# Kernel tuning notes

Measured on AMD Instinct MI355X. Metric: run time of the kernel, lower is better.

The kernel has to match this reference:

```python
import jax, jax.numpy as jnp
import numpy as np

B_, NWIN, WH, WW = 8, 256, 8, 8
DIM, HEADS = 192, 6
N = WH * WW


def setup_inputs() -> dict:
    key = jax.random.key(0)
    ks = jax.random.split(key, 5)
    return {
        "x": jax.random.normal(ks[0], (B_, NWIN, N, DIM), dtype=jnp.float32),
        "qkv_w": jax.random.normal(ks[1], (3 * DIM, DIM), dtype=jnp.float32) * 0.02,
        "qkv_b": jax.random.normal(ks[2], (3 * DIM,), dtype=jnp.float32) * 0.02,
        "proj_w": jax.random.normal(ks[3], (DIM, DIM), dtype=jnp.float32) * 0.02,
        "proj_b": jax.random.normal(ks[4], (DIM,), dtype=jnp.float32) * 0.02,
    }


def _grad_magnitude(t, B, H, n, d, Wh, Ww):
    # t: [B,H,n,N,d] -> spatial layout [B,H,n,d,Wh,Ww]
    t = jnp.swapaxes(t, 3, 4).reshape(B, H, n, d, Wh, Ww)
    # forward finite difference with zero pre-pad (matches conv2d [-1,1] pad=1 then slice)
    gx = t - jnp.concatenate([jnp.zeros_like(t[..., :1]), t[..., :-1]], axis=-1)
    gy = t - jnp.concatenate([jnp.zeros_like(t[..., :1, :]), t[..., :-1, :]], axis=-2)
    return jnp.sum(jnp.abs(gx) + jnp.abs(gy), axis=(-1, -2))  # [B,H,n,d]


def reference(x, qkv_w, qkv_b, proj_w, proj_b):
    B, n, Ntok, C = x.shape
    H = HEADS
    d = C // H
    scale = d ** (-0.5)
    qkv = x @ qkv_w.T + qkv_b                       # [B,n,N,3C]
    qkv = qkv.reshape(B, n, Ntok, 3, H, d)
    qkv = jnp.transpose(qkv, (3, 0, 4, 1, 2, 5))    # [3,B,H,n,N,d]
    q, k, v = qkv[0] * scale, qkv[1], qkv[2]
    qg = _grad_magnitude(q, B, H, n, d, WH, WW)     # [B,H,n,d]
    kg = _grad_magnitude(k, B, H, n, d, WH, WW)
    qg = jnp.swapaxes(qg, 2, 3)[..., None]          # [B,H,d,n,1]
    kg = jnp.swapaxes(kg, 2, 3)[..., None]          # [B,H,d,n,1]
    attn = qg @ jnp.swapaxes(kg, -1, -2)            # [B,H,d,n,n] rank-1 scores
    attn = jax.nn.softmax(attn, axis=-1)
    vp = jnp.transpose(v, (0, 1, 4, 2, 3))          # [B,H,d,n,N]
    out = attn @ vp                                 # [B,H,d,n,N]
    out = jnp.transpose(out, (0, 3, 4, 1, 2)).reshape(B * n, Ntok, C)
    return out @ proj_w.T + proj_b                  # [B*n, N, C]
```

## Files before the change

### kernel.cpp

```cpp
#include <hip/hip_runtime.h>
#include <cstddef>


#define SCALE 0.17677669529663687f

typedef __attribute__((ext_vector_type(8))) short short8;
typedef __attribute__((ext_vector_type(4))) float f32x4;

__device__ __forceinline__ unsigned short f2bf(float f) {
    unsigned u = __float_as_uint(f);
    u += 0x7fffu + ((u >> 16) & 1u);
    return (unsigned short)(u >> 16);
}
__device__ __forceinline__ float bf2f(unsigned int h) {
    return __uint_as_float(h << 16);
}
__device__ __forceinline__ unsigned pack2(unsigned short a, unsigned short b) {
    return (unsigned)a | ((unsigned)b << 16);
}

__global__ __launch_bounds__(256) void wsplit_kernel(
    const float* __restrict__ w, unsigned short* __restrict__ Wh,
    unsigned short* __restrict__ Wl)
{
    int idx = blockIdx.x * 256 + threadIdx.x;
    float v = w[idx];
    unsigned short h = f2bf(v);
    Wh[idx] = h;
    if (idx < 73728) Wl[idx] = f2bf(v - bf2f(h));
}

__global__ __launch_bounds__(256) void wproj_kernel(
    const float* __restrict__ w, unsigned short* __restrict__ Wp)
{
    int idx = blockIdx.x * 256 + threadIdx.x;
    Wp[idx] = f2bf(w[idx]);
}

__global__ __launch_bounds__(512, 2) void qkv_fused_kernel(
    const float* __restrict__ x, const unsigned short* __restrict__ Wh,
    const unsigned short* __restrict__ Wl, const float* __restrict__ bias,
    unsigned short* __restrict__ vT, float* __restrict__ qg, float* __restrict__ kg)
{
    __shared__ unsigned short As_h[2 * 128 * 32];
    __shared__ unsigned short As_l[2 * 128 * 32];

    const int tid = threadIdx.x;
    const int wave = tid >> 6, lane = tid & 63;
    const int quad = lane >> 4, col = lane & 15;
    const int wq = wave & 3;
    const int wofs4 = (wave >> 2) * 4;
    const int m0 = blockIdx.x * 128;

    const int arow = tid >> 2;
    const int apart = tid & 3;
    const float* xp = x + (size_t)(m0 + arow) * 192 + apart * 8;
    const int aslot = (((arow >> 4) * 64) + apart * 16 + (arow & 15)) * 8;

    const unsigned short* wh_base = Wh + (size_t)(wq * 16 + col) * 192 + quad * 8;
    const unsigned short* wl_base = Wl + (size_t)(wq * 16 + col) * 192 + quad * 8;

    f32x4 acc[9][4];
#pragma unroll
    for (int s = 0; s < 9; ++s)
#pragma unroll
        for (int mi = 0; mi < 4; ++mi) {
            f32x4 z = {0.f, 0.f, 0.f, 0.f};
            acc[s][mi] = z;
        }

    float4 pa0, pa1;
    auto load_chunk = [&](int kk) {
        pa0 = *(const float4*)(xp + kk * 32);
        pa1 = *(const float4*)(xp + kk * 32 + 4);
    };
    auto write_chunk = [&](int nb) {
        float v[8] = {pa0.x, pa0.y, pa0.z, pa0.w, pa1.x, pa1.y, pa1.z, pa1.w};
        unsigned short h[8], l[8];
#pragma unroll
        for (int i = 0; i < 8; ++i) {
            h[i] = f2bf(v[i]);
            l[i] = f2bf(v[i] - bf2f(h[i]));
        }
        uint4 H = make_uint4(pack2(h[0], h[1]), pack2(h[2], h[3]),
                             pack2(h[4], h[5]), pack2(h[6], h[7]));
        uint4 L = make_uint4(pack2(l[0], l[1]), pack2(l[2], l[3]),
                             pack2(l[4], l[5]), pack2(l[6], l[7]));
        *(uint4*)&As_h[nb * 4096 + aslot] = H;
        *(uint4*)&As_l[nb * 4096 + aslot] = L;
    };

    int ro8[4];
#pragma unroll
    for (int mi = 0; mi < 4; ++mi)
        ro8[mi] = ((wofs4 + mi) * 64 + quad * 16 + col) * 8;

    load_chunk(0);
    write_chunk(0);
    __syncthreads();

    for (int kk = 0; kk < 6; ++kk) {
        const int cur = kk & 1;
        if (kk < 5) load_chunk(kk + 1);

        const int kw = kk * 32;
        uint4 pbh[9], pbl[6];
#pragma unroll
        for (int s = 0; s < 9; ++s)
            pbh[s] = *(const uint4*)(wh_base + s * 12288 + kw);
#pragma unroll
        for (int s = 0; s < 6; ++s)
            pbl[s] = *(const uint4*)(wl_base + s * 12288 + kw);

        short8 ah[4], al[4];
#pragma unroll
        for (int mi = 0; mi < 4; ++mi) {
            ah[mi] = *(const short8*)&As_h[cur * 4096 + ro8[mi]];
            al[mi] = *(const short8*)&As_l[cur * 4096 + ro8[mi]];
        }

#pragma unroll
        for (int s = 0; s < 9; ++s) {
            short8 bh = *(const short8*)&pbh[s];
            if (s < 6) {
                short8 bl = *(const short8*)&pbl[s];
#pragma unroll
                for (int mi = 0; mi < 4; ++mi) {
                    acc[s][mi] = __builtin_amdgcn_mfma_f32_16x16x32_bf16(al[mi], bh, acc[s][mi], 0, 0, 0);
                    acc[s][mi] = __builtin_amdgcn_mfma_f32_16x16x32_bf16(ah[mi], bl, acc[s][mi], 0, 0, 0);
                    acc[s][mi] = __builtin_amdgcn_mfma_f32_16x16x32_bf16(ah[mi], bh, acc[s][mi], 0, 0, 0);
                }
            } else {
#pragma unroll
                for (int mi = 0; mi < 4; ++mi)
                    acc[s][mi] = __builtin_amdgcn_mfma_f32_16x16x32_bf16(ah[mi], bh, acc[s][mi], 0, 0, 0);
            }
        }

        if (kk < 5) write_chunk(1 - cur);
        __syncthreads();
    }

#pragma unroll
    for (int s = 0; s < 9; ++s) {
        float bv = bias[(wq + s * 4) * 16 + col];
#pragma unroll
        for (int mi = 0; mi < 4; ++mi)
#pragma unroll
            for (int r = 0; r < 4; ++r)
                acc[s][mi][r] += bv;
    }

    const int gw = blockIdx.x * 2 + (wave >> 2);
    const int b = gw >> 8, win = gw & 255;

#pragma unroll
    for (int s = 0; s < 6; ++s) {
        const int n = wq + s * 4;
        float yx[4][4], p3[4];
#pragma unroll
        for (int mi = 0; mi < 4; ++mi) {
#pragma unroll
            for (int r = 0; r < 4; ++r)
                yx[mi][r] = __shfl_xor(acc[s][mi][r], 32);
            p3[mi] = __shfl_xor(acc[s][mi][3], 16);
        }
        float sum = 0.f;
#pragma unroll
        for (int mi = 0; mi < 4; ++mi)
#pragma unroll
            for (int r = 0; r < 4; ++r) {
                float v = acc[s][mi][r];
                float gx = (r > 0) ? (v - acc[s][mi][r - 1])
                                   : ((quad & 1) ? (v - p3[mi]) : v);
                float gy = (quad >= 2) ? (v - yx[mi][r])
                                       : ((mi > 0) ? (v - yx[mi - 1][r]) : v);
                sum += fabsf(gx) + fabsf(gy);
            }
        sum += __shfl_xor(sum, 16);
        sum += __shfl_xor(sum, 32);
        float* dst = (s < 3) ? qg : kg;
        const int chb = ((s < 3) ? n : n - 12) * 16;
        const float sc = (s < 3) ? SCALE : 1.0f;
        if (lane < 16)
            dst[(size_t)(b * 192 + chb + lane) * 256 + win] = sum * sc;
    }
#pragma unroll
    for (int s = 6; s < 9; ++s) {
        const int ch = (wq + s * 4 - 24) * 16 + col;
#pragma unroll
        for (int mi = 0; mi < 4; ++mi) {
            int tok0 = mi * 16 + quad * 4;
            ushort4 o = make_ushort4(f2bf(acc[s][mi][0]), f2bf(acc[s][mi][1]),
                                     f2bf(acc[s][mi][2]), f2bf(acc[s][mi][3]));
            *(ushort4*)(vT + (size_t)(b * 192 + ch) * 16384 + win * 64 + tok0) = o;
        }
    }
}

__global__ __launch_bounds__(256) void attn_mfma_kernel(
    const unsigned short* __restrict__ vT, const float* __restrict__ qg,
    const float* __restrict__ kg, unsigned short* __restrict__ attbuf)
{
    __shared__ unsigned short Vs[64 * 264];
    __shared__ float kds[256];
    __shared__ float red[256];

    const int g = blockIdx.x;
    const int tid = threadIdx.x;
    const int wave = tid >> 6, lane = tid & 63;
    const int quad = lane >> 4, col = lane & 15;

    float kv = kg[(size_t)g * 256 + tid];
    red[tid] = kv;
    __syncthreads();
    for (int s = 128; s > 0; s >>= 1) {
        if (tid < s) red[tid] = fmaxf(red[tid], red[tid + s]);
        __syncthreads();
    }
    kds[tid] = kv - red[0];

    const unsigned short* vb = vT + (size_t)g * 16384;
    {
        const int jr = tid >> 3;
        const int tb = (tid & 7) * 8;
#pragma unroll
        for (int it = 0; it < 8; ++it) {
            int j = it * 32 + jr;
            uint4 u = *(const uint4*)(vb + (size_t)j * 64 + tb);
            Vs[(tb + 0) * 264 + j] = (unsigned short)(u.x & 0xffffu);
            Vs[(tb + 1) * 264 + j] = (unsigned short)(u.x >> 16);
            Vs[(tb + 2) * 264 + j] = (unsigned short)(u.y & 0xffffu);
            Vs[(tb + 3) * 264 + j] = (unsigned short)(u.y >> 16);
            Vs[(tb + 4) * 264 + j] = (unsigned short)(u.z & 0xffffu);
            Vs[(tb + 5) * 264 + j] = (unsigned short)(u.z >> 16);
            Vs[(tb + 6) * 264 + j] = (unsigned short)(u.w & 0xffffu);
            Vs[(tb + 7) * 264 + j] = (unsigned short)(u.w >> 16);
        }
    }

    float ai[4];
#pragma unroll
    for (int mi = 0; mi < 4; ++mi)
        ai[mi] = qg[(size_t)g * 256 + wave * 64 + mi * 16 + col];

    __syncthreads();

    f32x4 acc[4][4];
#pragma unroll
    for (int mi = 0; mi < 4; ++mi)
#pragma unroll
        for (int ni = 0; ni < 4; ++ni) {
            f32x4 z = {0.f, 0.f, 0.f, 0.f};
            acc[mi][ni] = z;
        }
    float den[4] = {0.f, 0.f, 0.f, 0.f};

    for (int kt = 0; kt < 8; ++kt) {
        const int k0 = kt * 32;
        float4 ka = *(const float4*)&kds[k0 + quad * 8];
        float4 kb = *(const float4*)&kds[k0 + quad * 8 + 4];
        float kv8[8] = {ka.x, ka.y, ka.z, ka.w, kb.x, kb.y, kb.z, kb.w};

        short8 bfr[4];
#pragma unroll
        for (int ni = 0; ni < 4; ++ni)
            bfr[ni] = *(const short8*)&Vs[(ni * 16 + col) * 264 + k0 + quad * 8];

#pragma unroll
        for (int mi = 0; mi < 4; ++mi) {
            short8 ef;
            float dl = 0.f;
#pragma unroll
            for (int j = 0; j < 8; ++j) {
                float e = __expf(ai[mi] * kv8[j]);
                unsigned short h = f2bf(e);
                ef[j] = (short)h;
                dl += bf2f(h);
            }
            den[mi] += dl;
#pragma unroll
            for (int ni = 0; ni < 4; ++ni)
                acc[mi][ni] = __builtin_amdgcn_mfma_f32_16x16x32_bf16(
                    ef, bfr[ni], acc[mi][ni], 0, 0, 0);
        }
    }

#pragma unroll
    for (int mi = 0; mi < 4; ++mi) {
        den[mi] += __shfl_xor(den[mi], 16);
        den[mi] += __shfl_xor(den[mi], 32);
    }

    unsigned short* ob = attbuf + (size_t)g * 16384;
#pragma unroll
    for (int mi = 0; mi < 4; ++mi) {
        float invr[4];
#pragma unroll
        for (int r = 0; r < 4; ++r)
            invr[r] = 1.0f / __shfl(den[mi], quad * 4 + r);
#pragma unroll
        for (int ni = 0; ni < 4; ++ni)
#pragma unroll
            for (int r = 0; r < 4; ++r) {
                int i = wave * 64 + mi * 16 + quad * 4 + r;
                int tok = ni * 16 + col;
                ob[i * 64 + tok] = f2bf(acc[mi][ni][r] * invr[r]);
            }
    }
}

__global__ __launch_bounds__(256) void proj_mfma_kernel(
    const unsigned short* __restrict__ attbuf, const unsigned short* __restrict__ Wp,
    const float* __restrict__ bias, float* __restrict__ out)
{
    __shared__ unsigned short Bs[64 * 40];
    __shared__ float T[32 * 197];

    const int tid = threadIdx.x;
    const int wave = tid >> 6, lane = tid & 63;
    const int quad = lane >> 4, col = lane & 15;
    const int rowg0 = blockIdx.x * 64;
    const int b = rowg0 >> 14;
    const int rl0 = rowg0 & 16383;
    const unsigned short* ab = attbuf + (size_t)b * 3145728;

    f32x4 acc[3][4];
#pragma unroll
    for (int mi = 0; mi < 3; ++mi)
#pragma unroll
        for (int ni = 0; ni < 4; ++ni) {
            f32x4 z = {0.f, 0.f, 0.f, 0.f};
            acc[mi][ni] = z;
        }

    const int chl = tid >> 3;
    const int rb = (tid & 7) * 8;

    for (int kt = 0; kt < 6; ++kt) {
        __syncthreads();
        {
            uint4 u = *(const uint4*)(ab + (size_t)(kt * 32 + chl) * 16384 + rl0 + rb);
            Bs[(rb + 0) * 40 + chl] = (unsigned short)(u.x & 0xffffu);
            Bs[(rb + 1) * 40 + chl] = (unsigned short)(u.x >> 16);
            Bs[(rb + 2) * 40 + chl] = (unsigned short)(u.y & 0xffffu);
            Bs[(rb + 3) * 40 + chl] = (unsigned short)(u.y >> 16);
            Bs[(rb + 4) * 40 + chl] = (unsigned short)(u.z & 0xffffu);
            Bs[(rb + 5) * 40 + chl] = (unsigned short)(u.z >> 16);
            Bs[(rb + 6) * 40 + chl] = (unsigned short)(u.w & 0xffffu);
            Bs[(rb + 7) * 40 + chl] = (unsigned short)(u.w >> 16);
        }
        __syncthreads();

        short8 bfr[4], af[3];
#pragma unroll
        for (int ni = 0; ni < 4; ++ni)
            bfr[ni] = *(const short8*)&Bs[(ni * 16 + col) * 40 + quad * 8];
#pragma unroll
        for (int mi = 0; mi < 3; ++mi)
            af[mi] = *(const short8*)(Wp + (size_t)(wave * 48 + mi * 16 + col) * 192
                                      + kt * 32 + quad * 8);
#pragma unroll
        for (int mi = 0; mi < 3; ++mi)
#pragma unroll
            for (int ni = 0; ni < 4; ++ni)
                acc[mi][ni] = __builtin_amdgcn_mfma_f32_16x16x32_bf16(
                    af[mi], bfr[ni], acc[mi][ni], 0, 0, 0);
    }

    float br[3][4];
#pragma unroll
    for (int mi = 0; mi < 3; ++mi)
#pragma unroll
        for (int r = 0; r < 4; ++r)
            br[mi][r] = bias[wave * 48 + mi * 16 + quad * 4 + r];

#pragma unroll
    for (int h = 0; h < 2; ++h) {
        __syncthreads();
#pragma unroll
        for (int nh = 0; nh < 2; ++nh) {
            int ni = h * 2 + nh;
#pragma unroll
            for (int mi = 0; mi < 3; ++mi)
#pragma unroll
                for (int r = 0; r < 4; ++r)
                    T[(nh * 16 + col) * 197 + wave * 48 + mi * 16 + quad * 4 + r] =
                        acc[mi][ni][r] + br[mi][r];
        }
        __syncthreads();
        {
            int row = tid >> 3;
            int ck = (tid & 7) * 24;
            float* op = out + (size_t)(rowg0 + h * 32 + row) * 192 + ck;
#pragma unroll
            for (int q4 = 0; q4 < 6; ++q4) {
                float4 o = make_float4(T[row * 197 + ck + q4 * 4 + 0],
                                       T[row * 197 + ck + q4 * 4 + 1],
                                       T[row * 197 + ck + q4 * 4 + 2],
                                       T[row * 197 + ck + q4 * 4 + 3]);
                *(float4*)(op + q4 * 4) = o;
            }
        }
    }
}

extern "C" void kernel_launch(void* const* d_in, const int* in_sizes, int n_in,
                              void* d_out, int out_size, void* d_ws, size_t ws_size,
                              hipStream_t stream) {
    const float* x      = (const float*)d_in[0];
    const float* qkv_w  = (const float*)d_in[1];
    const float* qkv_b  = (const float*)d_in[2];
    const float* proj_w = (const float*)d_in[3];
    const float* proj_b = (const float*)d_in[4];
    float* out = (float*)d_out;

    unsigned short* base16 = (unsigned short*)d_ws;
    unsigned short* vT16   = base16;
    unsigned short* attbuf = base16 + 25165824;
    float* qg = (float*)(base16 + 50331648);
    float* kg = qg + 393216;
    unsigned short* Wh = (unsigned short*)(kg + 393216);
    unsigned short* Wl = Wh + 110592;
    unsigned short* Wp = Wl + 73728;

    wsplit_kernel<<<432, 256, 0, stream>>>(qkv_w, Wh, Wl);
    wproj_kernel<<<144, 256, 0, stream>>>(proj_w, Wp);
    qkv_fused_kernel<<<1024, 512, 0, stream>>>(x, Wh, Wl, qkv_b, vT16, qg, kg);
    attn_mfma_kernel<<<1536, 256, 0, stream>>>(vT16, qg, kg, attbuf);
    proj_mfma_kernel<<<2048, 256, 0, stream>>>(attbuf, Wp, proj_b, out);
}
```

Measured before the change: 370.5 us.

## Restructure QKV kernel: one window per block, staged full-K LDS, grouped accumulators

The QKV projection kernel now handles one 64-token window per 256-thread block instead of two windows per 512-thread block. It loads the whole K=192 x tile into LDS once, replacing the double-buffered per-chunk pipeline and its per-iteration barriers. It also processes the 9 output slabs in three groups of 3 (q, k, v) with software-prefetched weight fragments, cutting live accumulators from 36 to 12 vectors so more waves fit per CU. The trade-off is more LDS per block, weights reloaded per group, and three sequential passes over the K loop.

After: 351.0 us. -5.2%, faster.

```diff
diff --git a/kernel.cpp b/kernel.cpp
--- a/kernel.cpp
+++ b/kernel.cpp
@@ -37,163 +37,173 @@
     Wp[idx] = f2bf(w[idx]);
 }
 
-__global__ __launch_bounds__(512, 2) void qkv_fused_kernel(
+__global__ __launch_bounds__(256, 3) void qkv_fused_kernel(
     const float* __restrict__ x, const unsigned short* __restrict__ Wh,
     const unsigned short* __restrict__ Wl, const float* __restrict__ bias,
     unsigned short* __restrict__ vT, float* __restrict__ qg, float* __restrict__ kg)
 {
-    __shared__ unsigned short As_h[2 * 128 * 32];
-    __shared__ unsigned short As_l[2 * 128 * 32];
+    __shared__ unsigned short As_h[6 * 2048];
+    __shared__ unsigned short As_l[6 * 2048];
 
     const int tid = threadIdx.x;
-    const int wave = tid >> 6, lane = tid & 63;
+    const int wq = tid >> 6, lane = tid & 63;
     const int quad = lane >> 4, col = lane & 15;
-    const int wq = wave & 3;
-    const int wofs4 = (wave >> 2) * 4;
-    const int m0 = blockIdx.x * 128;
-
-    const int arow = tid >> 2;
-    const int apart = tid & 3;
-    const float* xp = x + (size_t)(m0 + arow) * 192 + apart * 8;
-    const int aslot = (((arow >> 4) * 64) + apart * 16 + (arow & 15)) * 8;
+    const int gw = blockIdx.x;
+    const int b = gw >> 8, win = gw & 255;
+    const int m0 = gw * 64;
+
+    {
+        const int arow = tid >> 2;
+        const int apart = tid & 3;
+        const float* xp = x + (size_t)(m0 + arow) * 192 + apart * 8;
+        const int slot = (arow >> 4) * 512 + apart * 128 + (arow & 15) * 8;
+        float4 va[6], vb[6];
+#pragma unroll
+        for (int kk = 0; kk < 6; ++kk) {
+            va[kk] = *(const float4*)(xp + kk * 32);
+            vb[kk] = *(const float4*)(xp + kk * 32 + 4);
+        }
+#pragma unroll
+        for (int kk = 0; kk < 6; ++kk) {
+            float v[8] = {va[kk].x, va[kk].y, va[kk].z, va[kk].w,
+                          vb[kk].x, vb[kk].y, vb[kk].z, vb[kk].w};
+            unsigned short h[8], l[8];
+#pragma unroll
+            for (int i = 0; i < 8; ++i) {
+                h[i] = f2bf(v[i]);
+                l[i] = f2bf(v[i] - bf2f(h[i]));
+            }
+            uint4 H = make_uint4(pack2(h[0], h[1]), pack2(h[2], h[3]),
+                                 pack2(h[4], h[5]), pack2(h[6], h[7]));
+            uint4 L = make_uint4(pack2(l[0], l[1]), pack2(l[2], l[3]),
+                                 pack2(l[4], l[5]), pack2(l[6], l[7]));
+            *(uint4*)&As_h[kk * 2048 + slot] = H;
+            *(uint4*)&As_l[kk * 2048 + slot] = L;
+        }
+    }
+    __syncthreads();
 
     const unsigned short* wh_base = Wh + (size_t)(wq * 16 + col) * 192 + quad * 8;
     const unsigned short* wl_base = Wl + (size_t)(wq * 16 + col) * 192 + quad * 8;
 
-    f32x4 acc[9][4];
-#pragma unroll
-    for (int s = 0; s < 9; ++s)
-#pragma unroll
-        for (int mi = 0; mi < 4; ++mi) {
-            f32x4 z = {0.f, 0.f, 0.f, 0.f};
-            acc[s][mi] = z;
-        }
-
-    float4 pa0, pa1;
-    auto load_chunk = [&](int kk) {
-        pa0 = *(const float4*)(xp + kk * 32);
-        pa1 = *(const float4*)(xp + kk * 32 + 4);
-    };
-    auto write_chunk = [&](int nb) {
-        float v[8] = {pa0.x, pa0.y, pa0.z, pa0.w, pa1.x, pa1.y, pa1.z, pa1.w};
-        unsigned short h[8], l[8];
-#pragma unroll
-        for (int i = 0; i < 8; ++i) {
-            h[i] = f2bf(v[i]);
-            l[i] = f2bf(v[i] - bf2f(h[i]));
-        }
-        uint4 H = make_uint4(pack2(h[0], h[1]), pack2(h[2], h[3]),
-                             pack2(h[4], h[5]), pack2(h[6], h[7]));
-        uint4 L = make_uint4(pack2(l[0], l[1]), pack2(l[2], l[3]),
-                             pack2(l[4], l[5]), pack2(l[6], l[7]));
-        *(uint4*)&As_h[nb * 4096 + aslot] = H;
-        *(uint4*)&As_l[nb * 4096 + aslot] = L;
-    };
-
-    int ro8[4];
-#pragma unroll
-    for (int mi = 0; mi < 4; ++mi)
-        ro8[mi] = ((wofs4 + mi) * 64 + quad * 16 + col) * 8;
-
-    load_chunk(0);
-    write_chunk(0);
-    __syncthreads();
-
-    for (int kk = 0; kk < 6; ++kk) {
-        const int cur = kk & 1;
-        if (kk < 5) load_chunk(kk + 1);
-
-        const int kw = kk * 32;
-        uint4 pbh[9], pbl[6];
-#pragma unroll
-        for (int s = 0; s < 9; ++s)
-            pbh[s] = *(const uint4*)(wh_base + s * 12288 + kw);
-#pragma unroll
-        for (int s = 0; s < 6; ++s)
-            pbl[s] = *(const uint4*)(wl_base + s * 12288 + kw);
-
-        short8 ah[4], al[4];
-#pragma unroll
-        for (int mi = 0; mi < 4; ++mi) {
-            ah[mi] = *(const short8*)&As_h[cur * 4096 + ro8[mi]];
-            al[mi] = *(const short8*)&As_l[cur * 4096 + ro8[mi]];
-        }
-
-#pragma unroll
-        for (int s = 0; s < 9; ++s) {
-            short8 bh = *(const short8*)&pbh[s];
-            if (s < 6) {
-                short8 bl = *(const short8*)&pbl[s];
+#pragma unroll
+    for (int g = 0; g < 3; ++g) {
+        const bool qk = (g < 2);
+
+        f32x4 acc[3][4];
+#pragma unroll
+        for (int js = 0; js < 3; ++js)
+#pragma unroll
+            for (int mi = 0; mi < 4; ++mi) {
+                f32x4 z = {0.f, 0.f, 0.f, 0.f};
+                acc[js][mi] = z;
+            }
+
+        uint4 cbh[3], cbl[3], nbh[3], nbl[3];
+#pragma unroll
+        for (int js = 0; js < 3; ++js) {
+            const int s = g * 3 + js;
+            cbh[js] = *(const uint4*)(wh_base + (size_t)s * 12288);
+            if (qk) cbl[js] = *(const uint4*)(wl_base + (size_t)s * 12288);
+        }
+
+#pragma unroll
+        for (int kk = 0; kk < 6; ++kk) {
+            if (kk < 5) {
+#pragma unroll
+                for (int js = 0; js < 3; ++js) {
+                    const int s = g * 3 + js;
+                    nbh[js] = *(const uint4*)(wh_base + (size_t)s * 12288 + (kk + 1) * 32);
+                    if (qk) nbl[js] = *(const uint4*)(wl_base + (size_t)s * 12288 + (kk + 1) * 32);
+                }
+            }
+            short8 ah[4], al[4];
+#pragma unroll
+            for (int mi = 0; mi < 4; ++mi) {
+                ah[mi] = *(const short8*)&As_h[kk * 2048 + mi * 512 + lane * 8];
+                if (qk) al[mi] = *(const short8*)&As_l[kk * 2048 + mi * 512 + lane * 8];
+            }
+#pragma unroll
+            for (int js = 0; js < 3; ++js) {
+                short8 bh = *(const short8*)&cbh[js];
+                if (qk) {
+                    short8 bl = *(const short8*)&cbl[js];
+#pragma unroll
+                    for (int mi = 0; mi < 4; ++mi) {
+                        acc[js][mi] = __builtin_amdgcn_mfma_f32_16x16x32_bf16(al[mi], bh, acc[js][mi], 0, 0, 0);
+                        acc[js][mi] = __builtin_amdgcn_mfma_f32_16x16x32_bf16(ah[mi], bl, acc[js][mi], 0, 0, 0);
+                        acc[js][mi] = __builtin_amdgcn_mfma_f32_16x16x32_bf16(ah[mi], bh, acc[js][mi], 0, 0, 0);
+                    }
+                } else {
+#pragma unroll
+                    for (int mi = 0; mi < 4; ++mi)
+                        acc[js][mi] = __builtin_amdgcn_mfma_f32_16x16x32_bf16(ah[mi], bh, acc[js][mi], 0, 0, 0);
+                }
+            }
+#pragma unroll
+            for (int js = 0; js < 3; ++js) {
+                cbh[js] = nbh[js];
+                if (qk) cbl[js] = nbl[js];
+            }
+        }
+
+        if (g < 2) {
+#pragma unroll
+            for (int js = 0; js < 3; ++js) {
+                const int s = g * 3 + js;
+                const int n = wq + s * 4;
+                const float bv = bias[n * 16 + col];
+#pragma unroll
+                for (int mi = 0; mi < 4; ++mi)
+#pragma unroll
+                    for (int r = 0; r < 4; ++r)
+                        acc[js][mi][r] += bv;
+
+                float yx[4][4], p3[4];
 #pragma unroll
                 for (int mi = 0; mi < 4; ++mi) {
-                    acc[s][mi] = __builtin_amdgcn_mfma_f32_16x16x32_bf16(al[mi], bh, acc[s][mi], 0, 0, 0);
-                    acc[s][mi] = __builtin_amdgcn_mfma_f32_16x16x32_bf16(ah[mi], bl, acc[s][mi], 0, 0, 0);
-                    acc[s][mi] = __builtin_amdgcn_mfma_f32_16x16x32_bf16(ah[mi], bh, acc[s][mi], 0, 0, 0);
+#pragma unroll
+                    for (int r = 0; r < 4; ++r)
+                        yx[mi][r] = __shfl_xor(acc[js][mi][r], 32);
+                    p3[mi] = __shfl_xor(acc[js][mi][3], 16);
                 }
-            } else {
+                float sum = 0.f;
 #pragma unroll
                 for (int mi = 0; mi < 4; ++mi)
-                    acc[s][mi] = __builtin_amdgcn_mfma_f32_16x16x32_bf16(ah[mi], bh, acc[s][mi], 0, 0, 0);
-            }
-        }
-
-        if (kk < 5) write_chunk(1 - cur);
-        __syncthreads();
-    }
-
-#pragma unroll
-    for (int s = 0; s < 9; ++s) {
-        float bv = bias[(wq + s * 4) * 16 + col];
-#pragma unroll
-        for (int mi = 0; mi < 4; ++mi)
-#pragma unroll
-            for (int r = 0; r < 4; ++r)
-                acc[s][mi][r] += bv;
-    }
-
-    const int gw = blockIdx.x * 2 + (wave >> 2);
-    const int b = gw >> 8, win = gw & 255;
-
-#pragma unroll
-    for (int s = 0; s < 6; ++s) {
-        const int n = wq + s * 4;
-        float yx[4][4], p3[4];
-#pragma unroll
-        for (int mi = 0; mi < 4; ++mi) {
-#pragma unroll
-            for (int r = 0; r < 4; ++r)
-                yx[mi][r] = __shfl_xor(acc[s][mi][r], 32);
-            p3[mi] = __shfl_xor(acc[s][mi][3], 16);
-        }
-        float sum = 0.f;
-#pragma unroll
-        for (int mi = 0; mi < 4; ++mi)
-#pragma unroll
-            for (int r = 0; r < 4; ++r) {
-                float v = acc[s][mi][r];
-                float gx = (r > 0) ? (v - acc[s][mi][r - 1])
-                                   : ((quad & 1) ? (v - p3[mi]) : v);
-                float gy = (quad >= 2) ? (v - yx[mi][r])
-                                       : ((mi > 0) ? (v - yx[mi - 1][r]) : v);
-                sum += fabsf(gx) + fabsf(gy);
-            }
-        sum += __shfl_xor(sum, 16);
-        sum += __shfl_xor(sum, 32);
-        float* dst = (s < 3) ? qg : kg;
-        const int chb = ((s < 3) ? n : n - 12) * 16;
-        const float sc = (s < 3) ? SCALE : 1.0f;
-        if (lane < 16)
-            dst[(size_t)(b * 192 + chb + lane) * 256 + win] = sum * sc;
-    }
-#pragma unroll
-    for (int s = 6; s < 9; ++s) {
-        const int ch = (wq + s * 4 - 24) * 16 + col;
-#pragma unroll
-        for (int mi = 0; mi < 4; ++mi) {
-            int tok0 = mi * 16 + quad * 4;
-            ushort4 o = make_ushort4(f2bf(acc[s][mi][0]), f2bf(acc[s][mi][1]),
-                                     f2bf(acc[s][mi][2]), f2bf(acc[s][mi][3]));
-            *(ushort4*)(vT + (size_t)(b * 192 + ch) * 16384 + win * 64 + tok0) = o;
+#pragma unroll
+                    for (int r = 0; r < 4; ++r) {
+                        float v = acc[js][mi][r];
+                        float gx = (r > 0) ? (v - acc[js][mi][r - 1])
+                                           : ((quad & 1) ? (v - p3[mi]) : v);
+                        float gy = (quad >= 2) ? (v - yx[mi][r])
+                                               : ((mi > 0) ? (v - yx[mi - 1][r]) : v);
+                        sum += fabsf(gx) + fabsf(gy);
+                    }
+                sum += __shfl_xor(sum, 16);
+                sum += __shfl_xor(sum, 32);
+                float* dst = (g == 0) ? qg : kg;
+                const int chb = ((g == 0) ? n : n - 12) * 16;
+                const float sc = (g == 0) ? SCALE : 1.0f;
+                if (lane < 16)
+                    dst[(size_t)(b * 192 + chb + lane) * 256 + win] = sum * sc;
+            }
+        } else {
+#pragma unroll
+            for (int js = 0; js < 3; ++js) {
+                const int s = 6 + js;
+                const int n = wq + s * 4;
+                const float bv = bias[n * 16 + col];
+                const int ch = (n - 24) * 16 + col;
+#pragma unroll
+                for (int mi = 0; mi < 4; ++mi) {
+                    int tok0 = mi * 16 + quad * 4;
+                    ushort4 o = make_ushort4(f2bf(acc[js][mi][0] + bv),
+                                             f2bf(acc[js][mi][1] + bv),
+                                             f2bf(acc[js][mi][2] + bv),
+                                             f2bf(acc[js][mi][3] + bv));
+                    *(ushort4*)(vT + (size_t)(b * 192 + ch) * 16384 + win * 64 + tok0) = o;
+                }
+            }
         }
     }
 }
@@ -426,7 +436,7 @@
 
     wsplit_kernel<<<432, 256, 0, stream>>>(qkv_w, Wh, Wl);
     wproj_kernel<<<144, 256, 0, stream>>>(proj_w, Wp);
-    qkv_fused_kernel<<<1024, 512, 0, stream>>>(x, Wh, Wl, qkv_b, vT16, qg, kg);
+    qkv_fused_kernel<<<2048, 256, 0, stream>>>(x, Wh, Wl, qkv_b, vT16, qg, kg);
     attn_mfma_kernel<<<1536, 256, 0, stream>>>(vT16, qg, kg, attbuf);
     proj_mfma_kernel<<<2048, 256, 0, stream>>>(attbuf, Wp, proj_b, out);
 }
```

## Split QKV GEMM to one window per block with two M-halves per window

Applied to the files above, without the earlier changes.

Each block now handles a single 64-token window instead of two, with the two wave groups each computing half the window's rows. Cross-half gradient boundary rows and partial sums are exchanged through shared memory. The whole K dimension of x is staged into LDS up front, which removes the per-chunk double-buffer barriers. Weight fragments are loaded inside the MFMA loop instead of being prefetched. Halving the accumulator footprint raises the occupancy target to 4 blocks per CU and doubles the grid. The cost is reloading the weights twice as often per token and adding an extra barrier.

After: 522.5 us. +41.0%, slower.

```diff
diff --git a/kernel.cpp b/kernel.cpp
--- a/kernel.cpp
+++ b/kernel.cpp
@@ -37,163 +37,190 @@
     Wp[idx] = f2bf(w[idx]);
 }
 
-__global__ __launch_bounds__(512, 2) void qkv_fused_kernel(
+__global__ __launch_bounds__(512, 4) void qkv_fused_kernel(
     const float* __restrict__ x, const unsigned short* __restrict__ Wh,
     const unsigned short* __restrict__ Wl, const float* __restrict__ bias,
     unsigned short* __restrict__ vT, float* __restrict__ qg, float* __restrict__ kg)
 {
-    __shared__ unsigned short As_h[2 * 128 * 32];
-    __shared__ unsigned short As_l[2 * 128 * 32];
+    __shared__ unsigned short As_h[6 * 2048];
+    __shared__ unsigned short As_l[6 * 2048];
+    __shared__ float bnd[24][2][16][4];
+    __shared__ float ps[24][16];
 
     const int tid = threadIdx.x;
     const int wave = tid >> 6, lane = tid & 63;
     const int quad = lane >> 4, col = lane & 15;
-    const int wq = wave & 3;
-    const int wofs4 = (wave >> 2) * 4;
-    const int m0 = blockIdx.x * 128;
-
-    const int arow = tid >> 2;
-    const int apart = tid & 3;
-    const float* xp = x + (size_t)(m0 + arow) * 192 + apart * 8;
-    const int aslot = (((arow >> 4) * 64) + apart * 16 + (arow & 15)) * 8;
+    const int wq = wave & 3, mh = wave >> 2;
+    const int bid = blockIdx.x;
+    const int b = bid & 7, win = bid >> 3;
+    const int gw = b * 256 + win;
+    const int m0 = gw * 64;
+
+    {
+        const int khalf = tid >> 8;
+        const int t = tid & 255;
+        const int arow = t >> 2;
+        const int apart = t & 3;
+        const float* xp = x + (size_t)(m0 + arow) * 192 + apart * 8 + khalf * 96;
+        const int slot = (arow >> 4) * 512 + apart * 128 + (arow & 15) * 8;
+        float4 va[3], vb[3];
+#pragma unroll
+        for (int j = 0; j < 3; ++j) {
+            va[j] = *(const float4*)(xp + j * 32);
+            vb[j] = *(const float4*)(xp + j * 32 + 4);
+        }
+#pragma unroll
+        for (int j = 0; j < 3; ++j) {
+            const int kk = khalf * 3 + j;
+            float v[8] = {va[j].x, va[j].y, va[j].z, va[j].w,
+                          vb[j].x, vb[j].y, vb[j].z, vb[j].w};
+            unsigned short h[8], l[8];
+#pragma unroll
+            for (int i = 0; i < 8; ++i) {
+                h[i] = f2bf(v[i]);
+                l[i] = f2bf(v[i] - bf2f(h[i]));
+            }
+            uint4 H = make_uint4(pack2(h[0], h[1]), pack2(h[2], h[3]),
+                                 pack2(h[4], h[5]), pack2(h[6], h[7]));
+            uint4 L = make_uint4(pack2(l[0], l[1]), pack2(l[2], l[3]),
+                                 pack2(l[4], l[5]), pack2(l[6], l[7]));
+            *(uint4*)&As_h[kk * 2048 + slot] = H;
+            *(uint4*)&As_l[kk * 2048 + slot] = L;
+        }
+    }
+    __syncthreads();
 
     const unsigned short* wh_base = Wh + (size_t)(wq * 16 + col) * 192 + quad * 8;
     const unsigned short* wl_base = Wl + (size_t)(wq * 16 + col) * 192 + quad * 8;
 
-    f32x4 acc[9][4];
+    f32x4 acc[9][2];
 #pragma unroll
     for (int s = 0; s < 9; ++s)
 #pragma unroll
-        for (int mi = 0; mi < 4; ++mi) {
+        for (int ml = 0; ml < 2; ++ml) {
             f32x4 z = {0.f, 0.f, 0.f, 0.f};
-            acc[s][mi] = z;
-        }
-
-    float4 pa0, pa1;
-    auto load_chunk = [&](int kk) {
-        pa0 = *(const float4*)(xp + kk * 32);
-        pa1 = *(const float4*)(xp + kk * 32 + 4);
-    };
-    auto write_chunk = [&](int nb) {
-        float v[8] = {pa0.x, pa0.y, pa0.z, pa0.w, pa1.x, pa1.y, pa1.z, pa1.w};
-        unsigned short h[8], l[8];
-#pragma unroll
-        for (int i = 0; i < 8; ++i) {
-            h[i] = f2bf(v[i]);
-            l[i] = f2bf(v[i] - bf2f(h[i]));
-        }
-        uint4 H = make_uint4(pack2(h[0], h[1]), pack2(h[2], h[3]),
-                             pack2(h[4], h[5]), pack2(h[6], h[7]));
-        uint4 L = make_uint4(pack2(l[0], l[1]), pack2(l[2], l[3]),
-                             pack2(l[4], l[5]), pack2(l[6], l[7]));
-        *(uint4*)&As_h[nb * 4096 + aslot] = H;
-        *(uint4*)&As_l[nb * 4096 + aslot] = L;
-    };
-
-    int ro8[4];
-#pragma unroll
-    for (int mi = 0; mi < 4; ++mi)
-        ro8[mi] = ((wofs4 + mi) * 64 + quad * 16 + col) * 8;
-
-    load_chunk(0);
-    write_chunk(0);
-    __syncthreads();
-
+            acc[s][ml] = z;
+        }
+
+#pragma unroll
     for (int kk = 0; kk < 6; ++kk) {
-        const int cur = kk & 1;
-        if (kk < 5) load_chunk(kk + 1);
-
-        const int kw = kk * 32;
-        uint4 pbh[9], pbl[6];
-#pragma unroll
-        for (int s = 0; s < 9; ++s)
-            pbh[s] = *(const uint4*)(wh_base + s * 12288 + kw);
-#pragma unroll
-        for (int s = 0; s < 6; ++s)
-            pbl[s] = *(const uint4*)(wl_base + s * 12288 + kw);
-
-        short8 ah[4], al[4];
-#pragma unroll
-        for (int mi = 0; mi < 4; ++mi) {
-            ah[mi] = *(const short8*)&As_h[cur * 4096 + ro8[mi]];
-            al[mi] = *(const short8*)&As_l[cur * 4096 + ro8[mi]];
-        }
-
+        short8 ah[2], al[2];
+#pragma unroll
+        for (int ml = 0; ml < 2; ++ml) {
+            const int mi = mh * 2 + ml;
+            ah[ml] = *(const short8*)&As_h[kk * 2048 + mi * 512 + lane * 8];
+            al[ml] = *(const short8*)&As_l[kk * 2048 + mi * 512 + lane * 8];
+        }
 #pragma unroll
         for (int s = 0; s < 9; ++s) {
-            short8 bh = *(const short8*)&pbh[s];
+            uint4 wh4 = *(const uint4*)(wh_base + (size_t)s * 12288 + kk * 32);
+            short8 bh = *(const short8*)&wh4;
             if (s < 6) {
-                short8 bl = *(const short8*)&pbl[s];
-#pragma unroll
-                for (int mi = 0; mi < 4; ++mi) {
-                    acc[s][mi] = __builtin_amdgcn_mfma_f32_16x16x32_bf16(al[mi], bh, acc[s][mi], 0, 0, 0);
-                    acc[s][mi] = __builtin_amdgcn_mfma_f32_16x16x32_bf16(ah[mi], bl, acc[s][mi], 0, 0, 0);
-                    acc[s][mi] = __builtin_amdgcn_mfma_f32_16x16x32_bf16(ah[mi], bh, acc[s][mi], 0, 0, 0);
+                uint4 wl4 = *(const uint4*)(wl_base + (size_t)s * 12288 + kk * 32);
+                short8 bl = *(const short8*)&wl4;
+#pragma unroll
+                for (int ml = 0; ml < 2; ++ml) {
+                    acc[s][ml] = __builtin_amdgcn_mfma_f32_16x16x32_bf16(al[ml], bh, acc[s][ml], 0, 0, 0);
+                    acc[s][ml] = __builtin_amdgcn_mfma_f32_16x16x32_bf16(ah[ml], bl, acc[s][ml], 0, 0, 0);
+                    acc[s][ml] = __builtin_amdgcn_mfma_f32_16x16x32_bf16(ah[ml], bh, acc[s][ml], 0, 0, 0);
                 }
             } else {
 #pragma unroll
-                for (int mi = 0; mi < 4; ++mi)
-                    acc[s][mi] = __builtin_amdgcn_mfma_f32_16x16x32_bf16(ah[mi], bh, acc[s][mi], 0, 0, 0);
-            }
-        }
-
-        if (kk < 5) write_chunk(1 - cur);
-        __syncthreads();
+                for (int ml = 0; ml < 2; ++ml)
+                    acc[s][ml] = __builtin_amdgcn_mfma_f32_16x16x32_bf16(ah[ml], bh, acc[s][ml], 0, 0, 0);
+            }
+        }
     }
 
 #pragma unroll
     for (int s = 0; s < 9; ++s) {
-        float bv = bias[(wq + s * 4) * 16 + col];
-#pragma unroll
-        for (int mi = 0; mi < 4; ++mi)
+        const float bv = bias[(wq + s * 4) * 16 + col];
+#pragma unroll
+        for (int ml = 0; ml < 2; ++ml)
 #pragma unroll
             for (int r = 0; r < 4; ++r)
-                acc[s][mi][r] += bv;
-    }
-
-    const int gw = blockIdx.x * 2 + (wave >> 2);
-    const int b = gw >> 8, win = gw & 255;
-
-#pragma unroll
-    for (int s = 0; s < 6; ++s) {
-        const int n = wq + s * 4;
-        float yx[4][4], p3[4];
-#pragma unroll
-        for (int mi = 0; mi < 4; ++mi) {
-#pragma unroll
-            for (int r = 0; r < 4; ++r)
-                yx[mi][r] = __shfl_xor(acc[s][mi][r], 32);
-            p3[mi] = __shfl_xor(acc[s][mi][3], 16);
-        }
-        float sum = 0.f;
-#pragma unroll
-        for (int mi = 0; mi < 4; ++mi)
-#pragma unroll
-            for (int r = 0; r < 4; ++r) {
-                float v = acc[s][mi][r];
-                float gx = (r > 0) ? (v - acc[s][mi][r - 1])
-                                   : ((quad & 1) ? (v - p3[mi]) : v);
-                float gy = (quad >= 2) ? (v - yx[mi][r])
-                                       : ((mi > 0) ? (v - yx[mi - 1][r]) : v);
-                sum += fabsf(gx) + fabsf(gy);
-            }
-        sum += __shfl_xor(sum, 16);
-        sum += __shfl_xor(sum, 32);
-        float* dst = (s < 3) ? qg : kg;
-        const int chb = ((s < 3) ? n : n - 12) * 16;
-        const float sc = (s < 3) ? SCALE : 1.0f;
-        if (lane < 16)
-            dst[(size_t)(b * 192 + chb + lane) * 256 + win] = sum * sc;
-    }
+                acc[s][ml][r] += bv;
+    }
+
 #pragma unroll
     for (int s = 6; s < 9; ++s) {
         const int ch = (wq + s * 4 - 24) * 16 + col;
 #pragma unroll
-        for (int mi = 0; mi < 4; ++mi) {
-            int tok0 = mi * 16 + quad * 4;
-            ushort4 o = make_ushort4(f2bf(acc[s][mi][0]), f2bf(acc[s][mi][1]),
-                                     f2bf(acc[s][mi][2]), f2bf(acc[s][mi][3]));
+        for (int ml = 0; ml < 2; ++ml) {
+            const int tok0 = (mh * 2 + ml) * 16 + quad * 4;
+            ushort4 o = make_ushort4(f2bf(acc[s][ml][0]), f2bf(acc[s][ml][1]),
+                                     f2bf(acc[s][ml][2]), f2bf(acc[s][ml][3]));
             *(ushort4*)(vT + (size_t)(b * 192 + ch) * 16384 + win * 64 + tok0) = o;
+        }
+    }
+
+    if (mh == 0) {
+#pragma unroll
+        for (int s = 0; s < 6; ++s) {
+            if (quad >= 2) {
+#pragma unroll
+                for (int r = 0; r < 4; ++r)
+                    bnd[s * 4 + wq][quad - 2][col][r] = acc[s][1][r];
+            }
+            float yx[2][4], p3[2];
+#pragma unroll
+            for (int ml = 0; ml < 2; ++ml) {
+#pragma unroll
+                for (int r = 0; r < 4; ++r)
+                    yx[ml][r] = __shfl_xor(acc[s][ml][r], 32);
+                p3[ml] = __shfl_xor(acc[s][ml][3], 16);
+            }
+            float sum = 0.f;
+#pragma unroll
+            for (int ml = 0; ml < 2; ++ml)
+#pragma unroll
+                for (int r = 0; r < 4; ++r) {
+                    float v = acc[s][ml][r];
+                    float gx = (r > 0) ? (v - acc[s][ml][r - 1])
+                                       : ((quad & 1) ? (v - p3[ml]) : v);
+                    float gy = (quad >= 2) ? (v - yx[ml][r])
+                                           : ((ml == 1) ? (v - yx[0][r]) : v);
+                    sum += fabsf(gx) + fabsf(gy);
+                }
+            sum += __shfl_xor(sum, 16);
+            sum += __shfl_xor(sum, 32);
+            if (lane < 16) ps[s * 4 + wq][col] = sum;
+        }
+    }
+    __syncthreads();
+    if (mh == 1) {
+#pragma unroll
+        for (int s = 0; s < 6; ++s) {
+            float yx[2][4], p3[2];
+#pragma unroll
+            for (int ml = 0; ml < 2; ++ml) {
+#pragma unroll
+                for (int r = 0; r < 4; ++r)
+                    yx[ml][r] = __shfl_xor(acc[s][ml][r], 32);
+                p3[ml] = __shfl_xor(acc[s][ml][3], 16);
+            }
+            float sum = 0.f;
+#pragma unroll
+            for (int ml = 0; ml < 2; ++ml)
+#pragma unroll
+                for (int r = 0; r < 4; ++r) {
+                    float v = acc[s][ml][r];
+                    float gx = (r > 0) ? (v - acc[s][ml][r - 1])
+                                       : ((quad & 1) ? (v - p3[ml]) : v);
+                    float gy;
+                    if (quad >= 2) gy = v - yx[ml][r];
+                    else if (ml == 1) gy = v - yx[0][r];
+                    else gy = v - bnd[s * 4 + wq][quad][col][r];
+                    sum += fabsf(gx) + fabsf(gy);
+                }
+            sum += __shfl_xor(sum, 16);
+            sum += __shfl_xor(sum, 32);
+            const float total = sum + ps[s * 4 + wq][col];
+            float* dst = (s < 3) ? qg : kg;
+            const int chb = ((s < 3) ? (wq + s * 4) : (wq + (s - 3) * 4)) * 16;
+            const float sc = (s < 3) ? SCALE : 1.0f;
+            if (lane < 16)
+                dst[(size_t)(b * 192 + chb + lane) * 256 + win] = total * sc;
         }
     }
 }
@@ -426,7 +453,7 @@
 
     wsplit_kernel<<<432, 256, 0, stream>>>(qkv_w, Wh, Wl);
     wproj_kernel<<<144, 256, 0, stream>>>(proj_w, Wp);
-    qkv_fused_kernel<<<1024, 512, 0, stream>>>(x, Wh, Wl, qkv_b, vT16, qg, kg);
+    qkv_fused_kernel<<<2048, 512, 0, stream>>>(x, Wh, Wl, qkv_b, vT16, qg, kg);
     attn_mfma_kernel<<<1536, 256, 0, stream>>>(vT16, qg, kg, attbuf);
     proj_mfma_kernel<<<2048, 256, 0, stream>>>(attbuf, Wp, proj_b, out);
 }
```
